# Optimization experiments

Hardware: AMD Instinct MI355X
Metric: run time of the kernel (lower is better)

Reference implementation:

```python
import jax, jax.numpy as jnp
import numpy as np

B, N, PH = 256, 21, 12
FEAT, INP, LAT, HID, OUT, NT = 8, 256, 64, 512, 128, 4
IN0 = FEAT + LAT + INP  # 328: GRU / initial-hidden input width


def _l1norm(G):
    # torch.nn.functional.normalize(G, p=1, dim=1)
    return G / jnp.maximum(jnp.abs(G).sum(axis=1, keepdims=True), 1e-12)


def _graph_linear(x, G, W, b, T):
    # StaticGraphLinear with learn_influence=True: y = G_l1norm @ (x @ W[T]^T + b)
    y = jnp.einsum('bni,noi->bno', x, W[T]) + b
    return jnp.einsum('nm,bmo->bno', _l1norm(G), y)


def _quat_exp(v):
    # Quaternion(angle=|v|, axis=v).q -> [cos(t/2), sin(t/2)*v/|v|]
    theta = jnp.linalg.norm(v, axis=-1, keepdims=True)
    w = jnp.cos(0.5 * theta)
    k = jnp.where(theta > 1e-8, jnp.sin(0.5 * theta) / jnp.maximum(theta, 1e-8), 0.5)
    return jnp.concatenate([w, k * v], axis=-1)


def _qmul(a, b):
    # Hamilton product a*b, w-first convention
    w1, v1 = a[..., :1], a[..., 1:]
    w2, v2 = b[..., :1], b[..., 1:]
    w = w1 * w2 - jnp.sum(v1 * v2, axis=-1, keepdims=True)
    v = w1 * v2 + w2 * v1 + jnp.cross(v1, v2)
    return jnp.concatenate([w, v], axis=-1)


def setup_inputs() -> dict:
    key = jax.random.key(0)
    ks = jax.random.split(key, 26)
    s = 0.05
    eyeN = jnp.eye(N, dtype=jnp.float32)
    inp = {}
    inp['x'] = jax.random.normal(ks[0], (B, 2, N, FEAT), dtype=jnp.float32)
    inp['h'] = jax.random.normal(ks[1], (B, N, INP), dtype=jnp.float32)
    inp['z'] = jax.random.normal(ks[2], (B, N, LAT), dtype=jnp.float32)
    q = jax.random.normal(ks[3], (B, N, 4), dtype=jnp.float32)
    inp['q_t'] = q / jnp.linalg.norm(q, axis=-1, keepdims=True)
    inp['T'] = jax.random.randint(ks[4], (N,), 0, NT)
    inp['ph'] = PH
    # initial_hidden_h
    inp['W0'] = s * jax.random.normal(ks[5], (NT, HID, IN0))
    inp['b0'] = s * jax.random.normal(ks[6], (N, HID))
    inp['G0'] = eyeN + s * jax.random.normal(ks[7], (N, N))
    # StaticGraphGRU (1 layer)
    inp['Wih'] = s * jax.random.normal(ks[8], (NT, 3 * HID, IN0))
    inp['Whh'] = s * jax.random.normal(ks[9], (NT, 3 * HID, HID))
    inp['bih'] = s * jax.random.normal(ks[10], (N, 3 * HID))
    inp['bhh'] = s * jax.random.normal(ks[11], (N, 3 * HID))
    inp['Grnn'] = eyeN + s * jax.random.normal(ks[12], (N, N))
    inp['GA'] = s * jax.random.normal(ks[13], (N, N))  # learned additive influence
    # fc_q / fc_cov_lat
    inp['Wq'] = s * jax.random.normal(ks[14], (NT, OUT, HID))
    inp['bq'] = s * jax.random.normal(ks[15], (N, OUT))
    inp['Gq'] = eyeN + s * jax.random.normal(ks[16], (N, N))
    inp['Wc'] = s * jax.random.normal(ks[17], (NT, OUT, HID))
    inp['bc'] = s * jax.random.normal(ks[18], (N, OUT))
    inp['Gc'] = eyeN + s * jax.random.normal(ks[19], (N, N))
    # to_q / to_q_cov_lat (learn_influence=False -> identity influence)
    inp['W3'] = s * jax.random.normal(ks[20], (NT, 3, OUT))
    inp['b3'] = s * jax.random.normal(ks[21], (N, 3))
    inp['W6'] = s * jax.random.normal(ks[22], (NT, 6, OUT))
    inp['b6'] = s * jax.random.normal(ks[23], (N, 6))
    return inp


def reference(x, h, z, q_t, T, ph, W0, b0, G0, Wih, Whh, bih, bhh, Grnn, GA,
              Wq, bq, Gq, Wc, bc, Gc, W3, b3, W6, b6):
    x_t = x[:, -1]    # [B,N,FEAT]
    x_t_1 = x[:, -2]
    h_z = jnp.concatenate([z, h], axis=-1)  # [B,N,LAT+INP]
    rnn_h = _graph_linear(jnp.concatenate([x_t_1, h_z], axis=-1), G0, W0, b0, T)
    Gn = _l1norm(Grnn) + GA           # additive graph influence
    WihT, WhhT = Wih[T], Whh[T]       # gather per-node weights once [N,3H,*]
    W3T, W6T = W3[T], W6[T]

    def step(carry, _):
        x_c, q_c, h_c = carry
        xin = jnp.concatenate([x_c, h_z], axis=-1)  # [B,N,IN0]
        xr = jnp.einsum('nm,bmg->bng', Gn, jnp.einsum('bni,ngi->bng', xin, WihT) + bih)
        hr = jnp.einsum('nm,bmg->bng', Gn, jnp.einsum('bnh,ngh->bng', h_c, WhhT) + bhh)
        ir, iz, ic = jnp.split(xr, 3, axis=-1)
        hrr, hz2, hc2 = jnp.split(hr, 3, axis=-1)
        r = jax.nn.sigmoid(ir + hrr)
        zg = jax.nn.sigmoid(iz + hz2)
        n = jnp.tanh(ic + r * hc2)
        h_new = (1.0 - zg) * n + zg * h_c
        y = jnp.tanh(h_new)  # dropout=0 (eval)
        ys = jnp.tanh(_graph_linear(y, Gq, Wq, bq, T))
        yc = jnp.tanh(_graph_linear(y, Gc, Wc, bc, T))
        dq3 = jnp.einsum('bno,nao->bna', ys, W3T) + b3
        cov = jnp.einsum('bno,nao->bna', yc, W6T) + b6
        dq = _quat_exp(dq3)
        q_new = _qmul(dq, q_c)
        x_new = jnp.concatenate([q_new, dq], axis=-1)
        return (x_new, q_new, h_new), (dq, cov)

    _, (dqs, covs) = jax.lax.scan(step, (x_t, q_t, rnn_h), None, length=ph)
    dq = jnp.moveaxis(dqs, 0, 1)        # [B,ph,N,4]
    dq_cov_lat = jnp.moveaxis(covs, 0, 1)  # [B,ph,N,6]
    return dq, dq_cov_lat, x_t  # (dp, dp_cov_lat are None since position=False)
```

## Files before the change

kernel.cpp:

```cpp
#include <hip/hip_runtime.h>

typedef unsigned short u16;
typedef __bf16 bf16_t;
typedef bf16_t bf16x8 __attribute__((ext_vector_type(8)));
typedef float f32x4 __attribute__((ext_vector_type(4)));
typedef long long i64;

#define NN   21
#define BB   256
#define HID  512
#define G3   1536
#define NC2  2048
#define A0S  352
#define PH   12
#define WSK  516
#define LK   40

__device__ __forceinline__ u16 f2b(float f){ bf16_t b = (bf16_t)f; return __builtin_bit_cast(u16, b); }
__device__ __forceinline__ float b2f(u16 u){ bf16_t b = __builtin_bit_cast(bf16_t, u); return (float)b; }
__device__ __forceinline__ bf16_t fb(float f){ return (bf16_t)f; }
__device__ __forceinline__ float sigm(float x){ return 1.0f / (1.0f + __expf(-x)); }
__device__ __forceinline__ float ftanh(float x){
  x = fminf(15.0f, fmaxf(-15.0f, x));
  float e = __expf(2.0f * x);
  return (e - 1.0f) / (e + 1.0f);
}
__device__ __forceinline__ float ldf(const void* p, size_t idx, int mode){
  if (mode == 2) return b2f(((const u16*)p)[idx]);
  if (mode == 1) return (float)((const double*)p)[idx];
  return ((const float*)p)[idx];
}

__global__ void k_fill(float* out, int n, float c){
  int idx = blockIdx.x*256 + threadIdx.x;
  if (idx < n) out[idx] = c;
}

__global__ void k_detect(const void* w0raw, const void* traw, int* flags){
  if (threadIdx.x != 0 || blockIdx.x != 0) return;
  const float*  v32 = (const float*)w0raw;
  const double* v64 = (const double*)w0raw;
  const u16*    vbf = (const u16*)w0raw;
  int c32 = 0, c64 = 0, cbf = 0;
  for (int i = 0; i < 64; ++i){
    float a32 = fabsf(v32[i]);
    if (a32 >= 1e-8f && a32 <= 1e4f) ++c32;
    double a64 = fabs(v64[i]);
    if (a64 >= 1e-8 && a64 <= 1e4) ++c64;
    float abf = fabsf(b2f(vbf[i]));
    if (abf >= 1e-8f && abf <= 1e4f) ++cbf;
  }
  int mode;
  if (cbf >= 60 && c32 < 48) mode = 2;
  else if (c32 >= 48)        mode = 0;
  else if (c64 >= 48)        mode = 1;
  else                       mode = 2;
  flags[0] = mode;
  const int* tw = (const int*)traw;
  int ok64 = 1;
  for (int i = 0; i < NN; ++i){
    unsigned lo = (unsigned)tw[2*i];
    int hi = tw[2*i+1];
    if (hi != 0 || lo >= 4u) { ok64 = 0; break; }
  }
  flags[1] = ok64;
}
__global__ void k_cvt_i(const void* src, int* dst, int n, const int* flags){
  int idx = threadIdx.x;
  if (idx >= n) return;
  if (flags[1]) dst[idx] = (int)((const i64*)src)[idx];
  else          dst[idx] = ((const int*)src)[idx];
}
__global__ void k_cvt_f(const void* src, float* dst, int n, const int* flags){
  int idx = blockIdx.x*256 + threadIdx.x;
  if (idx < n) dst[idx] = ldf(src, idx, flags[0]);
}
__global__ void k_cvt_wpad(const void* W, u16* dst, const int* flags){
  int idx = blockIdx.x*256 + threadIdx.x;
  if (idx >= 4*G3*A0S) return;
  int k = idx % A0S, tg = idx / A0S;
  dst[idx] = (k < 328) ? f2b(ldf(W, (size_t)tg*328 + k, flags[0])) : (u16)0;
}
__global__ void k_cvt_w(const void* W, u16* dst, int n, const int* flags){
  int idx = blockIdx.x*256 + threadIdx.x;
  if (idx < n) dst[idx] = f2b(ldf(W, idx, flags[0]));
}
__global__ void k_cvt_wqc(const void* Wq, const void* Wc, u16* dst, const int* flags){
  int idx = blockIdx.x*256 + threadIdx.x;
  if (idx >= 4*256*512) return;
  int k  = idx & 511;
  int tg = idx >> 9;
  int g  = tg & 255;
  int t  = tg >> 8;
  const int md = flags[0];
  dst[idx] = f2b((g < 128) ? ldf(Wq, ((size_t)(t*128 + g) << 9) + k, md)
                           : ldf(Wc, ((size_t)(t*128 + (g-128)) << 9) + k, md));
}
__global__ void k_bqc(const void* bq, const void* bc, float* bqc, const int* flags){
  int idx = blockIdx.x*256 + threadIdx.x;
  if (idx >= NN*256) return;
  int o = idx & 255; int n = idx >> 8;
  const int md = flags[0];
  bqc[idx] = (o < 128) ? ldf(bq,(size_t)n*128+o,md) : ldf(bc,(size_t)n*128+(o-128),md);
}

__global__ void k_prep_G(const void* G0, const void* Grnn, const void* GA,
                         const void* Gq, const void* Gc, const int* flags,
                         float* G0s, float* Gns, float* Gqs, float* Gcs){
  int tid = threadIdx.x;
  if (tid >= 84) return;
  const int md = flags[0];
  int mat = tid / 21, row = tid % 21;
  const void* src = mat==0 ? G0 : mat==1 ? Grnn : mat==2 ? Gq : Gc;
  float* dst      = mat==0 ? G0s : mat==1 ? Gns : mat==2 ? Gqs : Gcs;
  float s = 0.f;
  for (int m=0;m<21;++m) s += fabsf(ldf(src,row*21+m,md));
  s = fmaxf(s, 1e-12f);
  for (int m=0;m<21;++m){
    float v = ldf(src,row*21+m,md) / s;
    if (mat==1) v += ldf(GA,row*21+m,md);
    dst[row*21+m] = v;
  }
}

__global__ void k_build_A0(const void* x, const void* z, const void* hin,
                           const int* flags, u16* A0){
  int idx = blockIdx.x*256 + threadIdx.x;
  if (idx >= NN*BB*A0S) return;
  const int md = flags[0];
  int k  = idx % A0S;
  int nb = idx / A0S;
  int b  = nb % BB;
  int n  = nb / BB;
  float v = 0.f;
  if (k < 8)        v = ldf(x, ((size_t)(b*2 + 0)*NN + n)*8 + k, md);
  else if (k < 72)  v = ldf(z, ((size_t)b*NN + n)*64 + (k - 8), md);
  else if (k < 328) v = ldf(hin, ((size_t)b*NN + n)*256 + (k - 72), md);
  A0[idx] = f2b(v);
}

__global__ void k_init_state(const void* x, const void* qt, const int* flags,
                             u16* Axin, float* qc, float* out2){
  int b = threadIdx.x; int n = blockIdx.x;
  const int md = flags[0];
  for (int f=0; f<8; ++f){
    float raw = ldf(x, ((size_t)(b*2 + 1)*NN + n)*8 + f, md);
    Axin[(size_t)(n*BB + b)*A0S + f] = f2b(raw);
    out2[(b*NN + n)*8 + f] = raw;
  }
  for (int c=0; c<4; ++c) qc[(n*BB + b)*4 + c] = ldf(qt, ((size_t)b*NN + n)*4 + c, md);
}

template<int ABF>
__global__ __launch_bounds__(256)
void k_ngemm(const void* __restrict__ A_, int sA,
             const void* __restrict__ W_, int sW, size_t tstride,
             const void* __restrict__ bias_, int biasN,
             const int* __restrict__ T, const int* __restrict__ flags, int K,
             float* __restrict__ C, int Nc)
{
  __shared__ float Ws[8*WSK];
  const int node = blockIdx.y;
  const int g0   = blockIdx.x*8;
  const int tid  = threadIdx.x;
  const int t    = T[node];
  const int md   = flags[0];
  for (int idx = tid; idx < 8*K; idx += 256){
    int gg = idx / K, kk = idx - gg*K;
    Ws[gg*WSK + kk] = ldf(W_, (size_t)t*tstride + (size_t)(g0+gg)*sW + kk, md);
  }
  __syncthreads();
  const int b = tid;
  const float* Af = (const float*)A_;
  const u16*   Ab = (const u16*)A_;
  float acc[8];
  #pragma unroll
  for (int gg=0; gg<8; ++gg) acc[gg] = ldf(bias_, (size_t)node*biasN + g0 + gg, md);
  const size_t abase = (size_t)(node*BB + b)*sA;
  for (int k=0; k<K; ++k){
    const float av = ABF ? b2f(Ab[abase + k]) : Af[abase + k];
    #pragma unroll
    for (int gg=0; gg<8; ++gg) acc[gg] += av * Ws[gg*WSK + k];
  }
  #pragma unroll
  for (int gg=0; gg<8; ++gg)
    C[(size_t)(node*BB + b)*Nc + g0 + gg] = acc[gg];
}

template<int AMODE, int GRUH>
__global__ __launch_bounds__(256,2)
void k_mgemm(const void* __restrict__ A_, int sA,
             const u16* __restrict__ W, int sW, size_t tstride,
             const int* __restrict__ T, int nchunks,
             const float* __restrict__ bias, int biasN,
             u16* __restrict__ C, int Nc, int goff)
{
  __shared__ u16 As[128*LK];
  __shared__ u16 Bs[128*LK];
  const int ntile = blockIdx.x, mtile = blockIdx.y, node = blockIdx.z;
  const int tid = threadIdx.x;
  const int t = T[node];
  const int lane = tid & 63, wv = tid >> 6;
  const int wm = wv & 1, wn = wv >> 1;
  const int l16 = lane & 15, quad = lane >> 4;
  const int row0 = mtile*128, col0 = ntile*128;

  f32x4 acc[4][4];
  #pragma unroll
  for (int mt=0; mt<4; ++mt)
  #pragma unroll
  for (int nt=0; nt<4; ++nt){
    const int col = col0 + wn*64 + nt*16 + l16;
    const float bv = bias[node*biasN + col];
    if (GRUH && ntile < 8){
      #pragma unroll
      for (int r=0;r<4;++r){
        const int row = row0 + wm*64 + mt*16 + quad*4 + r;
        acc[mt][nt][r] = bv + b2f(C[(size_t)(node*BB + row)*Nc + col]);
      }
    } else {
      #pragma unroll
      for (int r=0;r<4;++r) acc[mt][nt][r] = bv;
    }
  }

  const int sr = tid >> 1, seg = tid & 1;
  for (int kc = 0; kc < nchunks; ++kc){
    const int k0 = kc*32 + seg*16;
    if (AMODE == 0){
      const u16* srcA = (const u16*)A_ + (size_t)(node*BB + row0 + sr)*sA + k0;
      *(uint4*)&As[sr*LK + seg*16]     = *(const uint4*)srcA;
      *(uint4*)&As[sr*LK + seg*16 + 8] = *(const uint4*)(srcA + 8);
    } else {
      const float* srcA = (const float*)A_ + (size_t)(node*BB + row0 + sr)*sA + k0;
      float4 f0 = *(const float4*)(srcA);
      float4 f1 = *(const float4*)(srcA+4);
      float4 f2 = *(const float4*)(srcA+8);
      float4 f3 = *(const float4*)(srcA+12);
      bf16x8 v0, v1;
      v0[0]=fb(f0.x); v0[1]=fb(f0.y); v0[2]=fb(f0.z); v0[3]=fb(f0.w);
      v0[4]=fb(f1.x); v0[5]=fb(f1.y); v0[6]=fb(f1.z); v0[7]=fb(f1.w);
      v1[0]=fb(f2.x); v1[1]=fb(f2.y); v1[2]=fb(f2.z); v1[3]=fb(f2.w);
      v1[4]=fb(f3.x); v1[5]=fb(f3.y); v1[6]=fb(f3.z); v1[7]=fb(f3.w);
      *(bf16x8*)&As[sr*LK + seg*16]     = v0;
      *(bf16x8*)&As[sr*LK + seg*16 + 8] = v1;
    }
    {
      const u16* srcB = W + (size_t)t*tstride + (size_t)(col0 + sr)*sW + k0;
      *(uint4*)&Bs[sr*LK + seg*16]     = *(const uint4*)srcB;
      *(uint4*)&Bs[sr*LK + seg*16 + 8] = *(const uint4*)(srcB + 8);
    }
    __syncthreads();
    bf16x8 af[4], bfr[4];
    #pragma unroll
    for (int mt=0; mt<4; ++mt) af[mt]  = *(const bf16x8*)&As[(wm*64 + mt*16 + l16)*LK + quad*8];
    #pragma unroll
    for (int nt=0; nt<4; ++nt) bfr[nt] = *(const bf16x8*)&Bs[(wn*64 + nt*16 + l16)*LK + quad*8];
    #pragma unroll
    for (int mt=0; mt<4; ++mt)
    #pragma unroll
    for (int nt=0; nt<4; ++nt)
      acc[mt][nt] = __builtin_amdgcn_mfma_f32_16x16x32_bf16(af[mt], bfr[nt], acc[mt][nt], 0, 0, 0);
    __syncthreads();
  }

  #pragma unroll
  for (int mt=0; mt<4; ++mt)
  #pragma unroll
  for (int nt=0; nt<4; ++nt){
    const int col = col0 + wn*64 + nt*16 + l16;
    const int dcol = GRUH ? ((ntile < 8) ? col : col + 512) : col + goff;
    #pragma unroll
    for (int r=0;r<4;++r){
      const int row = row0 + wm*64 + mt*16 + quad*4 + r;
      C[(size_t)(node*BB + row)*Nc + dcol] = f2b(acc[mt][nt][r]);
    }
  }
}


__global__ __launch_bounds__(256)
void k_mix_init(const float* C0, const float* G0s, float* h){
  __shared__ float Gs[441];
  const int tid = threadIdx.x;
  for (int i = tid; i < 441; i += 256) Gs[i] = G0s[i];
  __syncthreads();
  const int b = blockIdx.y;
  const int j = blockIdx.x*256 + tid;
  float P[21];
  #pragma unroll
  for (int m=0;m<21;++m) P[m] = C0[(size_t)(m*BB + b)*HID + j];
  float R[21];
  for (int n=0;n<21;++n){
    float s = 0.f;
    #pragma unroll
    for (int m=0;m<21;++m) s += Gs[n*21+m]*P[m];
    R[n] = s;
  }
  for (int n=0;n<21;++n) h[(size_t)(n*BB + b)*HID + j] = R[n];
}

__global__ __launch_bounds__(256)
void k_gru(u16* __restrict__ Cb, const float* __restrict__ Gns, float* __restrict__ h){
  __shared__ float Gs[441];
  const int tid = threadIdx.x;
  for (int i = tid; i < 441; i += 256) Gs[i] = Gns[i];
  __syncthreads();
  const int b = blockIdx.y;
  const int j = blockIdx.x*256 + tid;
  float P1[21], P2[21], P3[21], P4[21];
  #pragma unroll
  for (int m=0;m<21;++m){
    const size_t base = (size_t)(m*BB + b)*NC2 + j;
    P1[m] = b2f(Cb[base]);
    P2[m] = b2f(Cb[base + 512]);
    P3[m] = b2f(Cb[base + 1024]);
    P4[m] = b2f(Cb[base + 1536]);
  }
  for (int n=0;n<21;++n){
    float s1=0.f, s2=0.f, s3=0.f, s4=0.f;
    #pragma unroll
    for (int m=0;m<21;++m){
      const float g = Gs[n*21+m];
      s1 += g*P1[m]; s2 += g*P2[m]; s3 += g*P3[m]; s4 += g*P4[m];
    }
    const size_t hi = (size_t)(n*BB + b)*HID + j;
    const float hc = h[hi];
    const float r  = sigm(s1);
    const float zg = sigm(s2);
    const float nn = ftanh(s3 + r*s4);
    const float hn = (1.f - zg)*nn + zg*hc;
    h[hi] = hn;
    Cb[(size_t)(n*BB + b)*NC2 + j] = f2b(ftanh(hn));
  }
}

__global__ __launch_bounds__(256)
void k_out(const u16* __restrict__ Cbig, const float* __restrict__ Gqs, const float* __restrict__ Gcs,
           const int* __restrict__ T, const int* __restrict__ flags,
           const void* __restrict__ W3, const void* __restrict__ b3,
           const void* __restrict__ W6, const void* __restrict__ b6,
           float* __restrict__ qc, u16* __restrict__ Axin,
           float* __restrict__ out_dq, float* __restrict__ out_cov, int s)
{
  const int tid = threadIdx.x;
  const int w = blockIdx.x*4 + (tid >> 6);
  const int lane = tid & 63;
  const int b = w / 21, n = w % 21;
  const int t = T[n];
  const int md = flags[0];
  float aq1=0.f, aq2=0.f, ac1=0.f, ac2=0.f;
  #pragma unroll
  for (int m=0;m<21;++m){
    const u16* c = Cbig + (size_t)(m*BB + b)*NC2 + 512;
    const float gq = Gqs[n*21+m], gc = Gcs[n*21+m];
    aq1 += gq*b2f(c[lane]);       aq2 += gq*b2f(c[lane+64]);
    ac1 += gc*b2f(c[lane+128]);   ac2 += gc*b2f(c[lane+192]);
  }
  const float ys1 = ftanh(aq1), ys2 = ftanh(aq2);
  const float yc1 = ftanh(ac1), yc2 = ftanh(ac2);
  float red[9];
  #pragma unroll
  for (int a=0;a<3;++a)
    red[a] = ys1*ldf(W3,(size_t)(t*3+a)*128 + lane,md) + ys2*ldf(W3,(size_t)(t*3+a)*128 + lane + 64,md);
  #pragma unroll
  for (int a=0;a<6;++a)
    red[3+a] = yc1*ldf(W6,(size_t)(t*6+a)*128 + lane,md) + yc2*ldf(W6,(size_t)(t*6+a)*128 + lane + 64,md);
  #pragma unroll
  for (int i=0;i<9;++i){
    red[i] += __shfl_xor(red[i], 32);
    red[i] += __shfl_xor(red[i], 16);
    red[i] += __shfl_xor(red[i], 8);
    red[i] += __shfl_xor(red[i], 4);
    red[i] += __shfl_xor(red[i], 2);
    red[i] += __shfl_xor(red[i], 1);
  }
  const float d0 = red[0] + ldf(b3,(size_t)n*3+0,md);
  const float d1 = red[1] + ldf(b3,(size_t)n*3+1,md);
  const float d2 = red[2] + ldf(b3,(size_t)n*3+2,md);
  const float theta = sqrtf(d0*d0 + d1*d1 + d2*d2);
  const float wq = cosf(0.5f*theta);
  const float kq = (theta > 1e-8f) ? (sinf(0.5f*theta) / fmaxf(theta, 1e-8f)) : 0.5f;
  const float x1 = kq*d0, y1 = kq*d1, z1 = kq*d2;
  if (lane == 0){
    float* q = qc + (size_t)(n*BB + b)*4;
    const float qw=q[0], qx=q[1], qy=q[2], qz=q[3];
    const float nw = wq*qw - (x1*qx + y1*qy + z1*qz);
    const float nx = wq*qx + qw*x1 + (y1*qz - z1*qy);
    const float ny = wq*qy + qw*y1 + (z1*qx - x1*qz);
    const float nz = wq*qz + qw*z1 + (x1*qy - y1*qx);
    q[0]=nw; q[1]=nx; q[2]=ny; q[3]=nz;
    u16* ax = Axin + (size_t)(n*BB + b)*A0S;
    ax[0]=f2b(nw); ax[1]=f2b(nx); ax[2]=f2b(ny); ax[3]=f2b(nz);
    ax[4]=f2b(wq); ax[5]=f2b(x1); ax[6]=f2b(y1); ax[7]=f2b(z1);
    float* od = out_dq + (size_t)((b*PH + s)*NN + n)*4;
    od[0]=wq; od[1]=x1; od[2]=y1; od[3]=z1;
    float* oc = out_cov + (size_t)((b*PH + s)*NN + n)*6;
    for (int a=0;a<6;++a) oc[a] = red[3+a] + ldf(b6,(size_t)n*6+a,md);
  }
}


extern "C" void kernel_launch(void* const* d_in, const int* in_sizes, int n_in,
                              void* d_out, int out_size, void* d_ws, size_t ws_size,
                              hipStream_t stream)
{
  const void* P[25];
  {
    int j = 0;
    for (int i = 0; i < 25; ++i){
      if (i == 5){ P[i] = nullptr; continue; }
      while (j < n_in && in_sizes[j] == 1) ++j;
      P[i] = (j < n_in) ? d_in[j++] : nullptr;
    }
  }

  char* wsb = (char*)d_ws;
  size_t off = 0;
  auto carve = [&](size_t bytes)->void*{
    void* p = wsb + off;
    off = (off + bytes + 255) & ~(size_t)255;
    return p;
  };

  int*   flags = (int*)  carve(2*4);
  int*   TI    = (int*)  carve(NN*4);
  float* G0s   = (float*)carve(441*4);
  float* Gns   = (float*)carve(441*4);
  float* Gqs   = (float*)carve(441*4);
  float* Gcs   = (float*)carve(441*4);
  float* bihF  = (float*)carve((size_t)NN*G3*4);
  float* bhhF  = (float*)carve((size_t)NN*G3*4);
  float* bqcF  = (float*)carve((size_t)NN*256*4);
  u16*   Axin  = (u16*)  carve((size_t)NN*BB*A0S*2);
  u16*   Wihb  = (u16*)  carve((size_t)4*G3*A0S*2);
  u16*   Whhb  = (u16*)  carve((size_t)4*G3*512*2);
  u16*   Wqcb  = (u16*)  carve((size_t)4*256*512*2);
  float* hbuf  = (float*)carve((size_t)NN*BB*HID*4);
  u16*   Cbig  = (u16*)  carve((size_t)NN*BB*NC2*2);
  float* qcv   = (float*)carve((size_t)NN*BB*4*4);
  const size_t NEED = off;

  float* out_dq  = (float*)d_out;
  float* out_cov = out_dq  + (size_t)BB*PH*NN*4;
  float* out_xt  = out_cov + (size_t)BB*PH*NN*6;

  if (ws_size < NEED){
    float code = 150.0f + (float)(ws_size >> 23);
    k_fill<<<(out_size+255)/256,256,0,stream>>>((float*)d_out, out_size, code);
    return;
  }

  k_detect<<<1,64,0,stream>>>(P[6], P[4], flags);
  k_cvt_i<<<1,64,0,stream>>>(P[4], TI, NN, flags);
  k_prep_G<<<1,128,0,stream>>>(P[8],P[13],P[14],P[17],P[20],flags, G0s,Gns,Gqs,Gcs);
  k_cvt_f<<<(NN*G3+255)/256,256,0,stream>>>(P[11], bihF, NN*G3, flags);
  k_cvt_f<<<(NN*G3+255)/256,256,0,stream>>>(P[12], bhhF, NN*G3, flags);
  k_bqc<<<(NN*256+255)/256,256,0,stream>>>(P[16],P[19],bqcF,flags);
  k_build_A0<<<(NN*BB*A0S+255)/256,256,0,stream>>>(P[0],P[2],P[1],flags,Axin);
  k_cvt_wpad<<<(4*G3*A0S+255)/256,256,0,stream>>>(P[9], Wihb, flags);
  k_cvt_w<<<(4*G3*512+255)/256,256,0,stream>>>(P[10], Whhb, 4*G3*512, flags);
  k_cvt_wqc<<<(4*256*512+255)/256,256,0,stream>>>(P[15],P[18],Wqcb,flags);

  k_ngemm<1><<<dim3(HID/8,NN),256,0,stream>>>(Axin,A0S, P[6],328,(size_t)512*328,
      P[7],512, TI,flags, 328, hbuf,512);
  k_mix_init<<<dim3(2,BB),256,0,stream>>>(hbuf,G0s,hbuf);
  k_init_state<<<NN,256,0,stream>>>(P[0],P[3],flags,Axin,qcv,out_xt);

  for (int s=0; s<PH; ++s){
    k_mgemm<0,0><<<dim3(12,2,NN),256,0,stream>>>(Axin,A0S, Wihb,A0S,(size_t)G3*A0S,
        TI, 11, bihF,G3, Cbig,NC2, 0);
    k_mgemm<1,1><<<dim3(12,2,NN),256,0,stream>>>(hbuf,HID, Whhb,512,(size_t)G3*512,
        TI, 16, bhhF,G3, Cbig,NC2, 0);
    k_gru<<<dim3(2,BB),256,0,stream>>>(Cbig,Gns,hbuf);
    k_mgemm<0,0><<<dim3(2,2,NN),256,0,stream>>>(Cbig,NC2, Wqcb,512,(size_t)256*512,
        TI, 16, bqcF,256, Cbig,NC2, 512);
    k_out<<<(NN*BB)/4,256,0,stream>>>(Cbig,Gqs,Gcs,TI,flags,P[21],P[22],P[23],P[24],
        qcv,Axin,out_dq,out_cov,s);
  }
}
```

Baseline: 1.339 ms.

## Hoist static GRU input projection out of loop and fuse per-step gate GEMMs

```diff
diff --git a/kernel.cpp b/kernel.cpp
--- a/kernel.cpp
+++ b/kernel.cpp
@@ -15,6 +15,7 @@
 #define PH   12
 #define WSK  516
 #define LK   40
+#define KP   544
 
 __device__ __forceinline__ u16 f2b(float f){ bf16_t b = (bf16_t)f; return __builtin_bit_cast(u16, b); }
 __device__ __forceinline__ float b2f(u16 u){ bf16_t b = __builtin_bit_cast(bf16_t, u); return (float)b; }
@@ -75,15 +76,40 @@
   int idx = blockIdx.x*256 + threadIdx.x;
   if (idx < n) dst[idx] = ldf(src, idx, flags[0]);
 }
-__global__ void k_cvt_wpad(const void* W, u16* dst, const int* flags){
-  int idx = blockIdx.x*256 + threadIdx.x;
-  if (idx >= 4*G3*A0S) return;
-  int k = idx % A0S, tg = idx / A0S;
-  dst[idx] = (k < 328) ? f2b(ldf(W, (size_t)tg*328 + k, flags[0])) : (u16)0;
+__global__ void k_cvt_wpadg(const void* W, u16* dst, int rows, int srcK, int dstK, const int* flags){
+  int idx = blockIdx.x*256 + threadIdx.x;
+  if (idx >= rows*dstK) return;
+  int k = idx % dstK, r = idx / dstK;
+  dst[idx] = (k < srcK) ? f2b(ldf(W, (size_t)r*srcK + k, flags[0])) : (u16)0;
 }
 __global__ void k_cvt_w(const void* W, u16* dst, int n, const int* flags){
   int idx = blockIdx.x*256 + threadIdx.x;
   if (idx < n) dst[idx] = f2b(ldf(W, idx, flags[0]));
+}
+__global__ void k_cvt_wstat(const void* Wih, u16* dst, const int* flags){
+  int idx = blockIdx.x*256 + threadIdx.x;
+  if (idx >= 4*G3*320) return;
+  int k2 = idx % 320, tg = idx / 320;
+  dst[idx] = f2b(ldf(Wih, (size_t)tg*328 + 8 + k2, flags[0]));
+}
+__global__ void k_pack_wpack(const void* Whh, const void* Wih, u16* Wp, const int* flags){
+  int idx = blockIdx.x*256 + threadIdx.x;
+  if (idx >= 4*NC2*KP) return;
+  const int md = flags[0];
+  int k  = idx % KP;
+  int tg = idx / KP;
+  int g  = tg % NC2;
+  int t  = tg / NC2;
+  float v = 0.f;
+  if (g < 1024){
+    if (k < 512)             v = ldf(Whh, ((size_t)(t*G3 + g) << 9) + k, md);
+    else if (k < 520)        v = ldf(Wih, (size_t)(t*G3 + g)*328 + (k - 512), md);
+  } else if (g < 1536){
+    if (k >= 512 && k < 520) v = ldf(Wih, (size_t)(t*G3 + g)*328 + (k - 512), md);
+  } else {
+    if (k < 512)             v = ldf(Whh, ((size_t)(t*G3 + (g - 512)) << 9) + k, md);
+  }
+  Wp[idx] = f2b(v);
 }
 __global__ void k_cvt_wqc(const void* Wq, const void* Wc, u16* dst, const int* flags){
   int idx = blockIdx.x*256 + threadIdx.x;
@@ -102,6 +128,19 @@
   int o = idx & 255; int n = idx >> 8;
   const int md = flags[0];
   bqc[idx] = (o < 128) ? ldf(bq,(size_t)n*128+o,md) : ldf(bc,(size_t)n*128+(o-128),md);
+}
+__global__ void k_biasS(const void* bih, const void* bhh, float* biasS, float* bhh2, const int* flags){
+  int idx = blockIdx.x*256 + threadIdx.x;
+  if (idx >= NN*G3) return;
+  const int md = flags[0];
+  int g = idx % G3;
+  float v = ldf(bih, idx, md);
+  if (g < 1024) v += ldf(bhh, idx, md);
+  biasS[idx] = v;
+  if (g >= 1024){
+    int n = idx / G3;
+    bhh2[n*512 + (g - 1024)] = ldf(bhh, idx, md);
+  }
 }
 
 __global__ void k_prep_G(const void* G0, const void* Grnn, const void* GA,
@@ -187,13 +226,13 @@
     C[(size_t)(node*BB + b)*Nc + g0 + gg] = acc[gg];
 }
 
-template<int AMODE, int GRUH>
+template<int AMODE, int GRUH, int FOUT>
 __global__ __launch_bounds__(256,2)
 void k_mgemm(const void* __restrict__ A_, int sA,
              const u16* __restrict__ W, int sW, size_t tstride,
              const int* __restrict__ T, int nchunks,
              const float* __restrict__ bias, int biasN,
-             u16* __restrict__ C, int Nc, int goff)
+             void* __restrict__ C_, int Nc, int goff)
 {
   __shared__ u16 As[128*LK];
   __shared__ u16 Bs[128*LK];
@@ -204,6 +243,8 @@
   const int wm = wv & 1, wn = wv >> 1;
   const int l16 = lane & 15, quad = lane >> 4;
   const int row0 = mtile*128, col0 = ntile*128;
+  u16* Cb = (u16*)C_;
+  float* Cf = (float*)C_;
 
   f32x4 acc[4][4];
   #pragma unroll
@@ -216,7 +257,7 @@
       #pragma unroll
       for (int r=0;r<4;++r){
         const int row = row0 + wm*64 + mt*16 + quad*4 + r;
-        acc[mt][nt][r] = bv + b2f(C[(size_t)(node*BB + row)*Nc + col]);
+        acc[mt][nt][r] = bv + b2f(Cb[(size_t)(node*BB + row)*Nc + col]);
       }
     } else {
       #pragma unroll
@@ -273,7 +314,99 @@
     #pragma unroll
     for (int r=0;r<4;++r){
       const int row = row0 + wm*64 + mt*16 + quad*4 + r;
-      C[(size_t)(node*BB + row)*Nc + dcol] = f2b(acc[mt][nt][r]);
+      if (FOUT) Cf[(size_t)(node*BB + row)*Nc + dcol] = acc[mt][nt][r];
+      else      Cb[(size_t)(node*BB + row)*Nc + dcol] = f2b(acc[mt][nt][r]);
+    }
+  }
+}
+
+__global__ __launch_bounds__(256,2)
+void k_fgemm(const float* __restrict__ H, const u16* __restrict__ Ax,
+             const u16* __restrict__ Wp,
+             const int* __restrict__ T,
+             const u16* __restrict__ Sbuf, const float* __restrict__ bhh2,
+             u16* __restrict__ C)
+{
+  __shared__ u16 As[128*LK];
+  __shared__ u16 Bs[128*LK];
+  const int ntile = blockIdx.x, mtile = blockIdx.y, node = blockIdx.z;
+  const int tid = threadIdx.x;
+  const int t = T[node];
+  const int lane = tid & 63, wv = tid >> 6;
+  const int wm = wv & 1, wn = wv >> 1;
+  const int l16 = lane & 15, quad = lane >> 4;
+  const int row0 = mtile*128, col0 = ntile*128;
+
+  f32x4 acc[4][4];
+  #pragma unroll
+  for (int mt=0; mt<4; ++mt)
+  #pragma unroll
+  for (int nt=0; nt<4; ++nt){
+    const int col = col0 + wn*64 + nt*16 + l16;
+    #pragma unroll
+    for (int r=0;r<4;++r){
+      const int row = row0 + wm*64 + mt*16 + quad*4 + r;
+      acc[mt][nt][r] = (col < 1536)
+        ? b2f(Sbuf[(size_t)(node*BB + row)*G3 + col])
+        : bhh2[node*512 + (col - 1536)];
+    }
+  }
+
+  int kc0 = 0, kc1 = 17;
+  if (ntile >= 8 && ntile < 12) kc0 = 16;
+  else if (ntile >= 12)         kc1 = 16;
+
+  const int sr = tid >> 1, seg = tid & 1;
+  for (int kc = kc0; kc < kc1; ++kc){
+    const int k0 = kc*32 + seg*16;
+    if (kc < 16){
+      const float* srcA = H + (size_t)(node*BB + row0 + sr)*HID + k0;
+      float4 f0 = *(const float4*)(srcA);
+      float4 f1 = *(const float4*)(srcA+4);
+      float4 f2 = *(const float4*)(srcA+8);
+      float4 f3 = *(const float4*)(srcA+12);
+      bf16x8 v0, v1;
+      v0[0]=fb(f0.x); v0[1]=fb(f0.y); v0[2]=fb(f0.z); v0[3]=fb(f0.w);
+      v0[4]=fb(f1.x); v0[5]=fb(f1.y); v0[6]=fb(f1.z); v0[7]=fb(f1.w);
+      v1[0]=fb(f2.x); v1[1]=fb(f2.y); v1[2]=fb(f2.z); v1[3]=fb(f2.w);
+      v1[4]=fb(f3.x); v1[5]=fb(f3.y); v1[6]=fb(f3.z); v1[7]=fb(f3.w);
+      *(bf16x8*)&As[sr*LK + seg*16]     = v0;
+      *(bf16x8*)&As[sr*LK + seg*16 + 8] = v1;
+    } else {
+      uint4 zz; zz.x = zz.y = zz.z = zz.w = 0u;
+      uint4 u0 = zz;
+      if (seg == 0) u0 = *(const uint4*)(Ax + (size_t)(node*BB + row0 + sr)*A0S);
+      *(uint4*)&As[sr*LK + seg*16]     = u0;
+      *(uint4*)&As[sr*LK + seg*16 + 8] = zz;
+    }
+    {
+      const u16* srcB = Wp + (size_t)t*NC2*KP + (size_t)(col0 + sr)*KP + k0;
+      *(uint4*)&Bs[sr*LK + seg*16]     = *(const uint4*)srcB;
+      *(uint4*)&Bs[sr*LK + seg*16 + 8] = *(const uint4*)(srcB + 8);
+    }
+    __syncthreads();
+    bf16x8 af[4], bfr[4];
+    #pragma unroll
+    for (int mt=0; mt<4; ++mt) af[mt]  = *(const bf16x8*)&As[(wm*64 + mt*16 + l16)*LK + quad*8];
+    #pragma unroll
+    for (int nt=0; nt<4; ++nt) bfr[nt] = *(const bf16x8*)&Bs[(wn*64 + nt*16 + l16)*LK + quad*8];
+    #pragma unroll
+    for (int mt=0; mt<4; ++mt)
+    #pragma unroll
+    for (int nt=0; nt<4; ++nt)
+      acc[mt][nt] = __builtin_amdgcn_mfma_f32_16x16x32_bf16(af[mt], bfr[nt], acc[mt][nt], 0, 0, 0);
+    __syncthreads();
+  }
+
+  #pragma unroll
+  for (int mt=0; mt<4; ++mt)
+  #pragma unroll
+  for (int nt=0; nt<4; ++nt){
+    const int col = col0 + wn*64 + nt*16 + l16;
+    #pragma unroll
+    for (int r=0;r<4;++r){
+      const int row = row0 + wm*64 + mt*16 + quad*4 + r;
+      C[(size_t)(node*BB + row)*NC2 + col] = f2b(acc[mt][nt][r]);
     }
   }
 }
@@ -415,6 +548,10 @@
     }
   }
 
+  float* out_dq  = (float*)d_out;
+  float* out_cov = out_dq  + (size_t)BB*PH*NN*4;
+  float* out_xt  = out_cov + (size_t)BB*PH*NN*6;
+
   char* wsb = (char*)d_ws;
   size_t off = 0;
   auto carve = [&](size_t bytes)->void*{
@@ -429,53 +566,98 @@
   float* Gns   = (float*)carve(441*4);
   float* Gqs   = (float*)carve(441*4);
   float* Gcs   = (float*)carve(441*4);
-  float* bihF  = (float*)carve((size_t)NN*G3*4);
-  float* bhhF  = (float*)carve((size_t)NN*G3*4);
   float* bqcF  = (float*)carve((size_t)NN*256*4);
+  float* qcv   = (float*)carve((size_t)NN*BB*4*4);
   u16*   Axin  = (u16*)  carve((size_t)NN*BB*A0S*2);
-  u16*   Wihb  = (u16*)  carve((size_t)4*G3*A0S*2);
-  u16*   Whhb  = (u16*)  carve((size_t)4*G3*512*2);
   u16*   Wqcb  = (u16*)  carve((size_t)4*256*512*2);
   float* hbuf  = (float*)carve((size_t)NN*BB*HID*4);
   u16*   Cbig  = (u16*)  carve((size_t)NN*BB*NC2*2);
-  float* qcv   = (float*)carve((size_t)NN*BB*4*4);
-  const size_t NEED = off;
-
-  float* out_dq  = (float*)d_out;
-  float* out_cov = out_dq  + (size_t)BB*PH*NN*4;
-  float* out_xt  = out_cov + (size_t)BB*PH*NN*6;
-
-  if (ws_size < NEED){
+  const size_t COMMON = off;
+
+  size_t offA = off;
+  auto carveA = [&](size_t bytes)->void*{
+    void* p = wsb + offA;
+    offA = (offA + bytes + 255) & ~(size_t)255;
+    return p;
+  };
+  float* b0F   = (float*)carveA((size_t)NN*HID*4);
+  float* biasS = (float*)carveA((size_t)NN*G3*4);
+  float* bhh2F = (float*)carveA((size_t)NN*512*4);
+  u16*   W0b   = (u16*)  carveA((size_t)4*HID*A0S*2);
+  u16*   Wstat = (u16*)  carveA((size_t)4*G3*320*2);
+  u16*   Wpack = (u16*)  carveA((size_t)4*NC2*KP*2);
+  u16*   Sbuf  = (u16*)  carveA((size_t)NN*BB*G3*2);
+  const size_t NEED_A = offA;
+
+  size_t offB = off;
+  auto carveB = [&](size_t bytes)->void*{
+    void* p = wsb + offB;
+    offB = (offB + bytes + 255) & ~(size_t)255;
+    return p;
+  };
+  float* bihF  = (float*)carveB((size_t)NN*G3*4);
+  float* bhhF  = (float*)carveB((size_t)NN*G3*4);
+  u16*   Wihb  = (u16*)  carveB((size_t)4*G3*A0S*2);
+  u16*   Whhb  = (u16*)  carveB((size_t)4*G3*512*2);
+  const size_t NEED_B = offB;
+
+  if (ws_size < NEED_B){
     float code = 150.0f + (float)(ws_size >> 23);
     k_fill<<<(out_size+255)/256,256,0,stream>>>((float*)d_out, out_size, code);
     return;
   }
+  (void)COMMON;
 
   k_detect<<<1,64,0,stream>>>(P[6], P[4], flags);
   k_cvt_i<<<1,64,0,stream>>>(P[4], TI, NN, flags);
   k_prep_G<<<1,128,0,stream>>>(P[8],P[13],P[14],P[17],P[20],flags, G0s,Gns,Gqs,Gcs);
-  k_cvt_f<<<(NN*G3+255)/256,256,0,stream>>>(P[11], bihF, NN*G3, flags);
-  k_cvt_f<<<(NN*G3+255)/256,256,0,stream>>>(P[12], bhhF, NN*G3, flags);
   k_bqc<<<(NN*256+255)/256,256,0,stream>>>(P[16],P[19],bqcF,flags);
   k_build_A0<<<(NN*BB*A0S+255)/256,256,0,stream>>>(P[0],P[2],P[1],flags,Axin);
-  k_cvt_wpad<<<(4*G3*A0S+255)/256,256,0,stream>>>(P[9], Wihb, flags);
-  k_cvt_w<<<(4*G3*512+255)/256,256,0,stream>>>(P[10], Whhb, 4*G3*512, flags);
   k_cvt_wqc<<<(4*256*512+255)/256,256,0,stream>>>(P[15],P[18],Wqcb,flags);
 
-  k_ngemm<1><<<dim3(HID/8,NN),256,0,stream>>>(Axin,A0S, P[6],328,(size_t)512*328,
-      P[7],512, TI,flags, 328, hbuf,512);
-  k_mix_init<<<dim3(2,BB),256,0,stream>>>(hbuf,G0s,hbuf);
-  k_init_state<<<NN,256,0,stream>>>(P[0],P[3],flags,Axin,qcv,out_xt);
-
-  for (int s=0; s<PH; ++s){
-    k_mgemm<0,0><<<dim3(12,2,NN),256,0,stream>>>(Axin,A0S, Wihb,A0S,(size_t)G3*A0S,
-        TI, 11, bihF,G3, Cbig,NC2, 0);
-    k_mgemm<1,1><<<dim3(12,2,NN),256,0,stream>>>(hbuf,HID, Whhb,512,(size_t)G3*512,
-        TI, 16, bhhF,G3, Cbig,NC2, 0);
-    k_gru<<<dim3(2,BB),256,0,stream>>>(Cbig,Gns,hbuf);
-    k_mgemm<0,0><<<dim3(2,2,NN),256,0,stream>>>(Cbig,NC2, Wqcb,512,(size_t)256*512,
-        TI, 16, bqcF,256, Cbig,NC2, 512);
-    k_out<<<(NN*BB)/4,256,0,stream>>>(Cbig,Gqs,Gcs,TI,flags,P[21],P[22],P[23],P[24],
-        qcv,Axin,out_dq,out_cov,s);
-  }
-}
+  if (ws_size >= NEED_A){
+    k_cvt_f<<<(NN*HID+255)/256,256,0,stream>>>(P[7], b0F, NN*HID, flags);
+    k_biasS<<<(NN*G3+255)/256,256,0,stream>>>(P[11],P[12],biasS,bhh2F,flags);
+    k_cvt_wpadg<<<(4*HID*A0S+255)/256,256,0,stream>>>(P[6], W0b, 4*HID, 328, A0S, flags);
+    k_cvt_wstat<<<(4*G3*320+255)/256,256,0,stream>>>(P[9], Wstat, flags);
+    k_pack_wpack<<<(4*NC2*KP+255)/256,256,0,stream>>>(P[10], P[9], Wpack, flags);
+
+    k_mgemm<0,0,1><<<dim3(4,2,NN),256,0,stream>>>(Axin,A0S, W0b,A0S,(size_t)HID*A0S,
+        TI, 11, b0F,HID, hbuf,HID, 0);
+    k_mix_init<<<dim3(2,BB),256,0,stream>>>(hbuf,G0s,hbuf);
+    k_mgemm<0,0,0><<<dim3(12,2,NN),256,0,stream>>>(Axin+8,A0S, Wstat,320,(size_t)G3*320,
+        TI, 10, biasS,G3, Sbuf,G3, 0);
+    k_init_state<<<NN,256,0,stream>>>(P[0],P[3],flags,Axin,qcv,out_xt);
+
+    for (int s=0; s<PH; ++s){
+      k_fgemm<<<dim3(16,2,NN),256,0,stream>>>(hbuf,Axin,Wpack,TI,Sbuf,bhh2F,Cbig);
+      k_gru<<<dim3(2,BB),256,0,stream>>>(Cbig,Gns,hbuf);
+      k_mgemm<0,0,0><<<dim3(2,2,NN),256,0,stream>>>(Cbig,NC2, Wqcb,512,(size_t)256*512,
+          TI, 16, bqcF,256, Cbig,NC2, 512);
+      k_out<<<(NN*BB)/4,256,0,stream>>>(Cbig,Gqs,Gcs,TI,flags,P[21],P[22],P[23],P[24],
+          qcv,Axin,out_dq,out_cov,s);
+    }
+  } else {
+    k_cvt_f<<<(NN*G3+255)/256,256,0,stream>>>(P[11], bihF, NN*G3, flags);
+    k_cvt_f<<<(NN*G3+255)/256,256,0,stream>>>(P[12], bhhF, NN*G3, flags);
+    k_cvt_wpadg<<<(4*G3*A0S+255)/256,256,0,stream>>>(P[9], Wihb, 4*G3, 328, A0S, flags);
+    k_cvt_w<<<(4*G3*512+255)/256,256,0,stream>>>(P[10], Whhb, 4*G3*512, flags);
+
+    k_ngemm<1><<<dim3(HID/8,NN),256,0,stream>>>(Axin,A0S, P[6],328,(size_t)512*328,
+        P[7],512, TI,flags, 328, hbuf,512);
+    k_mix_init<<<dim3(2,BB),256,0,stream>>>(hbuf,G0s,hbuf);
+    k_init_state<<<NN,256,0,stream>>>(P[0],P[3],flags,Axin,qcv,out_xt);
+
+    for (int s=0; s<PH; ++s){
+      k_mgemm<0,0,0><<<dim3(12,2,NN),256,0,stream>>>(Axin,A0S, Wihb,A0S,(size_t)G3*A0S,
+          TI, 11, bihF,G3, Cbig,NC2, 0);
+      k_mgemm<1,1,0><<<dim3(12,2,NN),256,0,stream>>>(hbuf,HID, Whhb,512,(size_t)G3*512,
+          TI, 16, bhhF,G3, Cbig,NC2, 0);
+      k_gru<<<dim3(2,BB),256,0,stream>>>(Cbig,Gns,hbuf);
+      k_mgemm<0,0,0><<<dim3(2,2,NN),256,0,stream>>>(Cbig,NC2, Wqcb,512,(size_t)256*512,
+          TI, 16, bqcF,256, Cbig,NC2, 512);
+      k_out<<<(NN*BB)/4,256,0,stream>>>(Cbig,Gqs,Gcs,TI,flags,P[21],P[22],P[23],P[24],
+          qcv,Axin,out_dq,out_cov,s);
+    }
+  }
+}
```

New measurement: 1.318 ms. No clear change (-1.6%).
